# Optimization experiments

Measured on AMD Instinct MI355X. Metric: run time of the kernel, lower is better.

The kernel has to match this reference:

```python
import jax, jax.numpy as jnp
import numpy as np


def _lgconv(x, row, col, num_nodes):
    # LGConv with normalize=True (gcn_norm, no self loops):
    # deg = in-degree on col; norm = deg^-1/2[row] * deg^-1/2[col]
    E = row.shape[0]
    deg = jax.ops.segment_sum(jnp.ones((E,), x.dtype), col, num_segments=num_nodes)
    dinv = jnp.where(deg > 0, jax.lax.rsqrt(jnp.maximum(deg, 1.0)), 0.0)
    norm = dinv[row] * dinv[col]                       # [E]
    msg = x[row] * norm[:, None]                       # gather + scale, [E, D]
    return jax.ops.segment_sum(msg, col, num_segments=num_nodes)  # scatter-add


def setup_inputs() -> dict:
    key = jax.random.key(0)
    k1, k2, k3 = jax.random.split(key, 3)
    NUM_NODES_GLOBAL = 1_000_000
    SUB_N = 100_000
    E = 1_600_000
    D = 64
    n_id = jax.random.randint(k1, (SUB_N,), 0, NUM_NODES_GLOBAL, dtype=jnp.int64 if jax.config.jax_enable_x64 else jnp.int32)
    edge_index = jax.random.randint(k2, (2, E), 0, SUB_N, dtype=jnp.int32)
    emb_weight = jax.random.normal(k3, (NUM_NODES_GLOBAL, D), dtype=jnp.float32) * 0.05
    return {"n_id": n_id, "edge_index": edge_index, "num_nodes": SUB_N, "emb_weight": emb_weight}


def reference(n_id, edge_index, num_nodes, emb_weight):
    NUM_LAYERS = 3
    row, col = edge_index[0], edge_index[1]
    x = emb_weight[n_id]                               # [N, D] embedding lookup
    acc = x
    cur = x
    for _ in range(NUM_LAYERS):
        cur = _lgconv(cur, row, col, num_nodes)
        acc = acc + cur
    return acc / (NUM_LAYERS + 1)                      # mean over stacked layers
```

## Files before the change

### kernel.cpp

```cpp
#include <hip/hip_runtime.h>
#include <hip/hip_fp16.h>


#define D 64
#define CAP 64
#define NBIN 1024
#define BINCAP 3072

typedef unsigned int u32;

__device__ inline __half2 u2h2(u32 u) { union { u32 i; __half2 h; } c; c.i = u; return c.h; }
__device__ inline u32 h22u(__half2 h) { union { u32 i; __half2 h; } c; c.h = h; return c.i; }

__global__ void zero_kernel(int4* __restrict__ p, int n4) {
    int i = blockIdx.x * blockDim.x + threadIdx.x;
    if (i < n4) p[i] = make_int4(0, 0, 0, 0);
}

__global__ void __launch_bounds__(1024) bink_kernel(const int* __restrict__ row,
                                                    const int* __restrict__ col,
                                                    int* __restrict__ bincur,
                                                    u32* __restrict__ binned, int E) {
    __shared__ u32 hist[NBIN];
    int tb = threadIdx.x;
    int chunk = (E + gridDim.x - 1) / gridDim.x;
    int s = blockIdx.x * chunk;
    int e = s + chunk; if (e > E) e = E;
    for (int i = tb; i < NBIN; i += 1024) hist[i] = 0;
    __syncthreads();
    for (int i = s + tb; i < e; i += 1024)
        atomicAdd(&hist[col[i] >> 7], 1u);
    __syncthreads();
    for (int b = tb; b < NBIN; b += 1024) {
        u32 c = hist[b];
        hist[b] = (c > 0) ? (u32)atomicAdd(&bincur[b], (int)c) : 0u;
    }
    __syncthreads();
    for (int i = s + tb; i < e; i += 1024) {
        int c = col[i];
        int b = c >> 7;
        u32 pos = atomicAdd(&hist[b], 1u);
        if (pos < BINCAP)
            __builtin_nontemporal_store(((u32)row[i] << 7) | (u32)(c & 127),
                                        &binned[(size_t)b * BINCAP + pos]);
    }
}

__global__ void __launch_bounds__(256) slot_kernel(const int* __restrict__ bincur,
                                                   const u32* __restrict__ binned,
                                                   int* __restrict__ rs,
                                                   int* __restrict__ cnt, int N) {
    __shared__ u32 rsbuf[128 * CAP];
    __shared__ u32 cur[128];
    int b = blockIdx.x;
    int t = threadIdx.x;
    if (t < 128) cur[t] = 0;
    __syncthreads();
    int c = bincur[b]; if (c > BINCAP) c = BINCAP;
    const u32* src = binned + (size_t)b * BINCAP;
    for (int i = t; i < c; i += 256) {
        u32 v = src[i];
        int nl = v & 127;
        u32 p = atomicAdd(&cur[nl], 1u);
        if (p < CAP) rsbuf[(nl << 6) + p] = v & 0xFFFFFF80u;
    }
    __syncthreads();
    uint4* dst = (uint4*)(rs + ((size_t)b << 13));
    const uint4* sb = (const uint4*)rsbuf;
    int nodebase = b << 7;
    for (int i = t; i < 2048; i += 256) {
        int node = nodebase + (i >> 4);
        if (node < N) dst[i] = sb[i];
    }
    if (t < 128) {
        int node = nodebase + t;
        if (node < N) cnt[node] = (int)(cur[t] < (u32)CAP ? cur[t] : (u32)CAP);
    }
}

__global__ void gather0_kernel(const int* __restrict__ n_id, const float4* __restrict__ emb,
                               const int* __restrict__ cnt, uint2* __restrict__ y,
                               float4* __restrict__ out, int N) {
    int t = blockIdx.x * blockDim.x + threadIdx.x;
    if (t >= N * 16) return;
    int i = t >> 4, q = t & 15;
    float4 v = emb[(size_t)n_id[i] * 16 + q];
    float4 o; o.x = 0.25f * v.x; o.y = 0.25f * v.y; o.z = 0.25f * v.z; o.w = 0.25f * v.w;
    out[(size_t)i * 16 + q] = o;
    int dg = cnt[i];
    float di = (dg > 0) ? rsqrtf((float)dg) : 0.0f;
    uint2 p;
    p.x = h22u(__floats2half2_rn(v.x * di, v.y * di));
    p.y = h22u(__floats2half2_rn(v.z * di, v.w * di));
    y[(size_t)i * 16 + q] = p;
}

template <bool WRITE_Y>
__global__ void layer_kernel(const int* __restrict__ cnt, const int* __restrict__ rs,
                             const char* __restrict__ y,
                             char* __restrict__ ynext,
                             float* __restrict__ out, int N) {
    int t = blockIdx.x * blockDim.x + threadIdx.x;
    int node = t >> 3;
    if (node >= N) return;
    int octoff = (t & 7) * 16;
    int dg = cnt[node];
    int e = (dg < CAP) ? dg : CAP;
    const int* rb = rs + ((size_t)node << 6);
    __half2 acc0 = __floats2half2_rn(0.f, 0.f), acc1 = acc0, acc2 = acc0, acc3 = acc0;
    int i = 0;
    for (; i + 1 < e; i += 2) {
        int off0 = rb[i];
        int off1 = rb[i + 1];
        uint4 w0 = *(const uint4*)(y + (size_t)off0 + octoff);
        uint4 w1 = *(const uint4*)(y + (size_t)off1 + octoff);
        acc0 = __hadd2(acc0, u2h2(w0.x)); acc1 = __hadd2(acc1, u2h2(w0.y));
        acc2 = __hadd2(acc2, u2h2(w0.z)); acc3 = __hadd2(acc3, u2h2(w0.w));
        acc0 = __hadd2(acc0, u2h2(w1.x)); acc1 = __hadd2(acc1, u2h2(w1.y));
        acc2 = __hadd2(acc2, u2h2(w1.z)); acc3 = __hadd2(acc3, u2h2(w1.w));
    }
    if (i < e) {
        uint4 w = *(const uint4*)(y + (size_t)rb[i] + octoff);
        acc0 = __hadd2(acc0, u2h2(w.x)); acc1 = __hadd2(acc1, u2h2(w.y));
        acc2 = __hadd2(acc2, u2h2(w.z)); acc3 = __hadd2(acc3, u2h2(w.w));
    }
    float di = (dg > 0) ? rsqrtf((float)dg) : 0.0f;
    float2 f0 = __half22float2(acc0);
    float2 f1 = __half22float2(acc1);
    float2 f2 = __half22float2(acc2);
    float2 f3 = __half22float2(acc3);
    float o[8] = { f0.x * di, f0.y * di, f1.x * di, f1.y * di,
                   f2.x * di, f2.y * di, f3.x * di, f3.y * di };
    float4* op = (float4*)(out + (size_t)node * D) + (octoff >> 3);
    float4 c0 = op[0], c1 = op[1];
    c0.x += 0.25f * o[0]; c0.y += 0.25f * o[1]; c0.z += 0.25f * o[2]; c0.w += 0.25f * o[3];
    c1.x += 0.25f * o[4]; c1.y += 0.25f * o[5]; c1.z += 0.25f * o[6]; c1.w += 0.25f * o[7];
    op[0] = c0; op[1] = c1;
    if (WRITE_Y) {
        uint4 w;
        w.x = h22u(__floats2half2_rn(o[0] * di, o[1] * di));
        w.y = h22u(__floats2half2_rn(o[2] * di, o[3] * di));
        w.z = h22u(__floats2half2_rn(o[4] * di, o[5] * di));
        w.w = h22u(__floats2half2_rn(o[6] * di, o[7] * di));
        *(uint4*)(ynext + (size_t)node * 128 + octoff) = w;
    }
}

extern "C" void kernel_launch(void* const* d_in, const int* in_sizes, int n_in,
                              void* d_out, int out_size, void* d_ws, size_t ws_size,
                              hipStream_t stream) {
    const int*    n_id = (const int*)d_in[0];
    const int*    edge = (const int*)d_in[1];
    const float*  emb  = (const float*)d_in[3];
    float* out = (float*)d_out;

    const int N = in_sizes[0];
    const int E = in_sizes[1] / 2;
    const int* row = edge;
    const int* col = edge + E;
    const int nbin = (N + 127) >> 7;

    char* p = (char*)d_ws;
    auto alloc = [&](size_t bytes) { char* r = p; p += (bytes + 255) & ~(size_t)255; return r; };
    int*  bincur = (int*) alloc((size_t)NBIN * 4);
    u32*  binned = (u32*) alloc((size_t)nbin * BINCAP * 4);
    int*  cnt    = (int*) alloc((size_t)nbin * 128 * 4);
    int*  rs     = (int*) alloc((size_t)nbin * 128 * CAP * 4);
    char* yA     = (char*)alloc((size_t)N * D * 2);
    char* yB     = (char*)alloc((size_t)N * D * 2);

    const int BS = 256;

    zero_kernel<<<1, BS, 0, stream>>>((int4*)bincur, NBIN / 4);
    bink_kernel<<<128, 1024, 0, stream>>>(row, col, bincur, binned, E);
    slot_kernel<<<nbin, BS, 0, stream>>>(bincur, binned, rs, cnt, N);

    gather0_kernel<<<((size_t)N * 16 + BS - 1) / BS, BS, 0, stream>>>(
        n_id, (const float4*)emb, cnt, (uint2*)yA, (float4*)out, N);

    const int LG = ((size_t)N * 8 + BS - 1) / BS;
    layer_kernel<true ><<<LG, BS, 0, stream>>>(cnt, rs, yA, yB, out, N);
    layer_kernel<true ><<<LG, BS, 0, stream>>>(cnt, rs, yB, yA, out, N);
    layer_kernel<false><<<LG, BS, 0, stream>>>(cnt, rs, yA, yB, out, N);
}
```

Before: 192.2 us.

## Fuse embedding gather and three propagation layers into one cooperative kernel

Replaces the gather kernel and the three per-layer kernels with a single cooperative launch. Each thread owns up to four (node, octet) items and keeps the running layer sum in registers across layers, using grid.sync between layers. This removes the per-layer read-modify-write of the fp32 output array and three launch gaps. In exchange, far fewer threads are resident, each processing several gather lists one after another, which may reduce memory-level parallelism on latency-bound gathers. The degree is also no longer clamped to CAP when it sets the loop bound.

```diff
diff --git a/kernel.cpp b/kernel.cpp
--- a/kernel.cpp
+++ b/kernel.cpp
@@ -1,11 +1,15 @@
 #include <hip/hip_runtime.h>
 #include <hip/hip_fp16.h>
+#include <hip/hip_cooperative_groups.h>
+
+namespace cg = cooperative_groups;
 
 
 #define D 64
 #define CAP 64
 #define NBIN 1024
 #define BINCAP 3072
+#define MAXOWN 4
 
 typedef unsigned int u32;
 
@@ -78,71 +82,99 @@
     }
 }
 
-__global__ void gather0_kernel(const int* __restrict__ n_id, const float4* __restrict__ emb,
-                               const int* __restrict__ cnt, uint2* __restrict__ y,
-                               float4* __restrict__ out, int N) {
-    int t = blockIdx.x * blockDim.x + threadIdx.x;
-    if (t >= N * 16) return;
-    int i = t >> 4, q = t & 15;
-    float4 v = emb[(size_t)n_id[i] * 16 + q];
-    float4 o; o.x = 0.25f * v.x; o.y = 0.25f * v.y; o.z = 0.25f * v.z; o.w = 0.25f * v.w;
-    out[(size_t)i * 16 + q] = o;
-    int dg = cnt[i];
-    float di = (dg > 0) ? rsqrtf((float)dg) : 0.0f;
-    uint2 p;
-    p.x = h22u(__floats2half2_rn(v.x * di, v.y * di));
-    p.y = h22u(__floats2half2_rn(v.z * di, v.w * di));
-    y[(size_t)i * 16 + q] = p;
-}
-
-template <bool WRITE_Y>
-__global__ void layer_kernel(const int* __restrict__ cnt, const int* __restrict__ rs,
-                             const char* __restrict__ y,
-                             char* __restrict__ ynext,
-                             float* __restrict__ out, int N) {
-    int t = blockIdx.x * blockDim.x + threadIdx.x;
-    int node = t >> 3;
-    if (node >= N) return;
-    int octoff = (t & 7) * 16;
-    int dg = cnt[node];
-    int e = (dg < CAP) ? dg : CAP;
-    const int* rb = rs + ((size_t)node << 6);
-    __half2 acc0 = __floats2half2_rn(0.f, 0.f), acc1 = acc0, acc2 = acc0, acc3 = acc0;
-    int i = 0;
-    for (; i + 1 < e; i += 2) {
-        int off0 = rb[i];
-        int off1 = rb[i + 1];
-        uint4 w0 = *(const uint4*)(y + (size_t)off0 + octoff);
-        uint4 w1 = *(const uint4*)(y + (size_t)off1 + octoff);
-        acc0 = __hadd2(acc0, u2h2(w0.x)); acc1 = __hadd2(acc1, u2h2(w0.y));
-        acc2 = __hadd2(acc2, u2h2(w0.z)); acc3 = __hadd2(acc3, u2h2(w0.w));
-        acc0 = __hadd2(acc0, u2h2(w1.x)); acc1 = __hadd2(acc1, u2h2(w1.y));
-        acc2 = __hadd2(acc2, u2h2(w1.z)); acc3 = __hadd2(acc3, u2h2(w1.w));
-    }
-    if (i < e) {
-        uint4 w = *(const uint4*)(y + (size_t)rb[i] + octoff);
-        acc0 = __hadd2(acc0, u2h2(w.x)); acc1 = __hadd2(acc1, u2h2(w.y));
-        acc2 = __hadd2(acc2, u2h2(w.z)); acc3 = __hadd2(acc3, u2h2(w.w));
-    }
-    float di = (dg > 0) ? rsqrtf((float)dg) : 0.0f;
-    float2 f0 = __half22float2(acc0);
-    float2 f1 = __half22float2(acc1);
-    float2 f2 = __half22float2(acc2);
-    float2 f3 = __half22float2(acc3);
-    float o[8] = { f0.x * di, f0.y * di, f1.x * di, f1.y * di,
-                   f2.x * di, f2.y * di, f3.x * di, f3.y * di };
-    float4* op = (float4*)(out + (size_t)node * D) + (octoff >> 3);
-    float4 c0 = op[0], c1 = op[1];
-    c0.x += 0.25f * o[0]; c0.y += 0.25f * o[1]; c0.z += 0.25f * o[2]; c0.w += 0.25f * o[3];
-    c1.x += 0.25f * o[4]; c1.y += 0.25f * o[5]; c1.z += 0.25f * o[6]; c1.w += 0.25f * o[7];
-    op[0] = c0; op[1] = c1;
-    if (WRITE_Y) {
+__global__ void __launch_bounds__(256, 4) fused_kernel(
+        const int* __restrict__ n_id, const float4* __restrict__ emb,
+        const int* __restrict__ cnt, const int* __restrict__ rs,
+        char* __restrict__ yA, char* __restrict__ yB,
+        float* __restrict__ out, int N) {
+    cg::grid_group grid = cg::this_grid();
+    const int gsz = gridDim.x * blockDim.x;
+    const int tid = blockIdx.x * blockDim.x + threadIdx.x;
+    const int total = N * 8;
+
+    int    ownIdx[MAXOWN];
+    int    ownE  [MAXOWN];
+    float  ownDi [MAXOWN];
+    float4 oa0[MAXOWN], oa1[MAXOWN];
+    int nown = 0;
+
+    for (int idx = tid; idx < total && nown < MAXOWN; idx += gsz) {
+        int node = idx >> 3, oct = idx & 7;
+        int dg = cnt[node];
+        float di = (dg > 0) ? rsqrtf((float)dg) : 0.0f;
+        ownIdx[nown] = idx;
+        ownE[nown]   = dg;
+        ownDi[nown]  = di;
+        const float4* ep = emb + (size_t)n_id[node] * 16 + oct * 2;
+        float4 v0 = ep[0], v1 = ep[1];
+        oa0[nown] = v0; oa1[nown] = v1;
         uint4 w;
-        w.x = h22u(__floats2half2_rn(o[0] * di, o[1] * di));
-        w.y = h22u(__floats2half2_rn(o[2] * di, o[3] * di));
-        w.z = h22u(__floats2half2_rn(o[4] * di, o[5] * di));
-        w.w = h22u(__floats2half2_rn(o[6] * di, o[7] * di));
-        *(uint4*)(ynext + (size_t)node * 128 + octoff) = w;
+        w.x = h22u(__floats2half2_rn(v0.x * di, v0.y * di));
+        w.y = h22u(__floats2half2_rn(v0.z * di, v0.w * di));
+        w.z = h22u(__floats2half2_rn(v1.x * di, v1.y * di));
+        w.w = h22u(__floats2half2_rn(v1.z * di, v1.w * di));
+        *(uint4*)(yA + (size_t)node * 128 + oct * 16) = w;
+        ++nown;
+    }
+
+    char* ys = yA;
+    char* yd = yB;
+    for (int layer = 0; layer < 3; ++layer) {
+        grid.sync();
+        #pragma unroll
+        for (int k = 0; k < MAXOWN; ++k) {
+            if (k >= nown) break;
+            int idx = ownIdx[k];
+            int node = idx >> 3, octoff = (idx & 7) * 16;
+            int e = ownE[k];
+            const int* rb = rs + ((size_t)node << 6);
+            __half2 acc0 = __floats2half2_rn(0.f, 0.f), acc1 = acc0, acc2 = acc0, acc3 = acc0;
+            int i = 0;
+            for (; i + 1 < e; i += 2) {
+                int off0 = rb[i];
+                int off1 = rb[i + 1];
+                uint4 w0 = *(const uint4*)(ys + (size_t)off0 + octoff);
+                uint4 w1 = *(const uint4*)(ys + (size_t)off1 + octoff);
+                acc0 = __hadd2(acc0, u2h2(w0.x)); acc1 = __hadd2(acc1, u2h2(w0.y));
+                acc2 = __hadd2(acc2, u2h2(w0.z)); acc3 = __hadd2(acc3, u2h2(w0.w));
+                acc0 = __hadd2(acc0, u2h2(w1.x)); acc1 = __hadd2(acc1, u2h2(w1.y));
+                acc2 = __hadd2(acc2, u2h2(w1.z)); acc3 = __hadd2(acc3, u2h2(w1.w));
+            }
+            if (i < e) {
+                uint4 w = *(const uint4*)(ys + (size_t)rb[i] + octoff);
+                acc0 = __hadd2(acc0, u2h2(w.x)); acc1 = __hadd2(acc1, u2h2(w.y));
+                acc2 = __hadd2(acc2, u2h2(w.z)); acc3 = __hadd2(acc3, u2h2(w.w));
+            }
+            float di = ownDi[k];
+            float2 f0 = __half22float2(acc0);
+            float2 f1 = __half22float2(acc1);
+            float2 f2 = __half22float2(acc2);
+            float2 f3 = __half22float2(acc3);
+            float o0 = f0.x * di, o1 = f0.y * di, o2 = f1.x * di, o3 = f1.y * di;
+            float o4 = f2.x * di, o5 = f2.y * di, o6 = f3.x * di, o7 = f3.y * di;
+            oa0[k].x += o0; oa0[k].y += o1; oa0[k].z += o2; oa0[k].w += o3;
+            oa1[k].x += o4; oa1[k].y += o5; oa1[k].z += o6; oa1[k].w += o7;
+            if (layer < 2) {
+                uint4 w;
+                w.x = h22u(__floats2half2_rn(o0 * di, o1 * di));
+                w.y = h22u(__floats2half2_rn(o2 * di, o3 * di));
+                w.z = h22u(__floats2half2_rn(o4 * di, o5 * di));
+                w.w = h22u(__floats2half2_rn(o6 * di, o7 * di));
+                *(uint4*)(yd + (size_t)node * 128 + octoff) = w;
+            }
+        }
+        char* t = ys; ys = yd; yd = t;
+    }
+
+    #pragma unroll
+    for (int k = 0; k < MAXOWN; ++k) {
+        if (k >= nown) break;
+        int idx = ownIdx[k];
+        int node = idx >> 3, oct = idx & 7;
+        float4* op = (float4*)(out + (size_t)node * D) + oct * 2;
+        float4 r0 = oa0[k], r1 = oa1[k];
+        op[0] = make_float4(0.25f * r0.x, 0.25f * r0.y, 0.25f * r0.z, 0.25f * r0.w);
+        op[1] = make_float4(0.25f * r1.x, 0.25f * r1.y, 0.25f * r1.z, 0.25f * r1.w);
     }
 }
 
@@ -175,11 +207,10 @@
     bink_kernel<<<128, 1024, 0, stream>>>(row, col, bincur, binned, E);
     slot_kernel<<<nbin, BS, 0, stream>>>(bincur, binned, rs, cnt, N);
 
-    gather0_kernel<<<((size_t)N * 16 + BS - 1) / BS, BS, 0, stream>>>(
-        n_id, (const float4*)emb, cnt, (uint2*)yA, (float4*)out, N);
-
-    const int LG = ((size_t)N * 8 + BS - 1) / BS;
-    layer_kernel<true ><<<LG, BS, 0, stream>>>(cnt, rs, yA, yB, out, N);
-    layer_kernel<true ><<<LG, BS, 0, stream>>>(cnt, rs, yB, yA, out, N);
-    layer_kernel<false><<<LG, BS, 0, stream>>>(cnt, rs, yA, yB, out, N);
-}
+    int total = N * 8;
+    int nblk = (total + BS * MAXOWN - 1) / (BS * MAXOWN);
+    void* args[] = { (void*)&n_id, (void*)&emb, (void*)&cnt, (void*)&rs,
+                     (void*)&yA, (void*)&yB, (void*)&out, (void*)&N };
+    hipLaunchCooperativeKernel((const void*)fused_kernel,
+                               dim3(nblk), dim3(BS), args, 0, stream);
+}
```

New measurement: 493.4 us. +156.8%, slower.
